# Kernel optimization log

Measured on AMD Instinct MI355X. Metric: run time of the kernel, lower is better.

## Reference

```python
import jax, jax.numpy as jnp
import numpy as np

IN_DIM, H1, H2, N_CLS, N_DOM = 7, 64, 128, 9, 2
N_S, E_S = 100000, 3200000
N_C, E_C = 512, 16384


def gcn_conv(x, edge_index, W, b):
    # PyG GCNConv: x' = D^{-1/2} (A + I) D^{-1/2} (x W) + b
    N = x.shape[0]
    h = x @ W
    loops = jnp.arange(N)
    row = jnp.concatenate([edge_index[0], loops])  # sources
    col = jnp.concatenate([edge_index[1], loops])  # targets
    deg = jax.ops.segment_sum(jnp.ones_like(col, dtype=h.dtype), col, num_segments=N)
    dis = jnp.where(deg > 0, jax.lax.rsqrt(deg), 0.0)
    norm = dis[row] * dis[col]
    out = jax.ops.segment_sum(h[row] * norm[:, None], col, num_segments=N)
    return out + b


def setup_inputs() -> dict:
    key = jax.random.key(0)
    ks = jax.random.split(key, 24)
    d = {}
    d['x_s'] = jax.random.normal(ks[0], (N_S, IN_DIM), dtype=jnp.float32)
    d['x_c'] = jax.random.normal(ks[1], (N_C, IN_DIM), dtype=jnp.float32)
    d['Q'] = jax.random.uniform(ks[2], (N_S, N_C), dtype=jnp.float32)
    d['edge_index_s'] = jax.random.randint(ks[3], (2, E_S), 0, N_S)
    d['edge_index_c'] = jax.random.randint(ks[4], (2, E_C), 0, N_C)
    s = 0.1
    d['W1s'] = jax.random.normal(ks[5], (IN_DIM, H1)) * s
    d['b1s'] = jnp.zeros((H1,), jnp.float32)
    d['W2s'] = jax.random.normal(ks[6], (H1, H2)) * s
    d['b2s'] = jnp.zeros((H2,), jnp.float32)
    d['W1c'] = jax.random.normal(ks[7], (IN_DIM, H1)) * s
    d['b1c'] = jnp.zeros((H1,), jnp.float32)
    d['W2c'] = jax.random.normal(ks[8], (H1, H2)) * s
    d['b2c'] = jnp.zeros((H2,), jnp.float32)
    d['A1'] = jax.random.normal(ks[9], (2 * H2, H2)) * s
    d['ab1'] = jnp.zeros((H2,), jnp.float32)
    d['A2'] = jax.random.normal(ks[10], (H2, 2)) * s
    d['ab2'] = jnp.zeros((2,), jnp.float32)
    d['Wcls'] = jax.random.normal(ks[11], (H2, N_CLS)) * s
    d['bcls'] = jnp.zeros((N_CLS,), jnp.float32)
    d['D1'] = jax.random.normal(ks[12], (H2, H1)) * s
    d['db1'] = jnp.zeros((H1,), jnp.float32)
    d['D2'] = jax.random.normal(ks[13], (H1, N_DOM)) * s
    d['db2'] = jnp.zeros((N_DOM,), jnp.float32)
    return d


def reference(x_s, x_c, Q, edge_index_s, edge_index_c,
              W1s, b1s, W2s, b2s, W1c, b1c, W2c, b2c,
              A1, ab1, A2, ab2, Wcls, bcls, D1, db1, D2, db2):
    # sample branch (eval mode: dropout is identity)
    xs = jax.nn.relu(gcn_conv(x_s, edge_index_s, W1s, b1s))
    xs = jax.nn.relu(gcn_conv(xs, edge_index_s, W2s, b2s))
    # cluster branch
    xc = jax.nn.relu(gcn_conv(x_c, edge_index_c, W1c, b1c))
    xc = jax.nn.relu(gcn_conv(xc, edge_index_c, W2c, b2c))
    # cross-graph decode
    xc_dec = Q @ xc  # [N_s, 128]
    fusion = jnp.concatenate([xs, xc_dec], axis=1)  # [N_s, 256]
    w = jax.nn.softmax(jax.nn.relu(fusion @ A1 + ab1) @ A2 + ab2, axis=1)
    fused = w[:, 0:1] * xs + w[:, 1:2] * xc_dec
    class_output = fused @ Wcls + bcls
    # gradient reversal is identity in forward
    domain_output = jax.nn.relu(fused @ D1 + db1) @ D2 + db2
    return (class_output, domain_output, fused)
```

## Files before the change

### kernel.cpp

```cpp
#include <hip/hip_runtime.h>
#include <cstdint>
#include <cstddef>

static constexpr int kNS = 100000;
static constexpr int kNC = 512;
static constexpr int kES = 3200000;
static constexpr int kEC = 16384;

static constexpr int kNB = (kNS + 63) / 64;
static constexpr int kNB8 = kNB * 8;
static constexpr int kCHUNK = 8192;
static constexpr int kNBLK = (kES + kCHUNK - 1) / kCHUNK;

static constexpr int kGemmQBlocks = (kNS + 63) / 64;
static constexpr int kAgg64Blocks = (kNS + 7) / 8;
static constexpr int kG1 = 625;
static constexpr int kG2 = 469;
static constexpr int kG3 = kGemmQBlocks - kG1 - kG2;

typedef __attribute__((ext_vector_type(8))) short short8;
typedef __attribute__((ext_vector_type(4))) float f32x4;

__device__ __forceinline__ unsigned short f2bf(float f) {
  union { float f; unsigned u; } v; v.f = f;
  unsigned u = v.u;
  unsigned r = (u + 0x7fffu + ((u >> 16) & 1u)) >> 16;
  return (unsigned short)r;
}
__device__ __forceinline__ float bflo(unsigned v) { return __uint_as_float(v << 16); }
__device__ __forceinline__ float bfhi(unsigned v) { return __uint_as_float(v & 0xffff0000u); }
__device__ __forceinline__ float bf2f(unsigned short s) { return __uint_as_float(((unsigned)s) << 16); }

__global__ __launch_bounds__(256) void k_passA(const int* __restrict__ col, int E,
                                               int* __restrict__ counts) {
  __shared__ int hist[kNB];
  int t = threadIdx.x, bid = blockIdx.x;
  for (int j = t; j < kNB; j += 256) hist[j] = 0;
  __syncthreads();
  int base = bid * kCHUNK;
#pragma unroll 4
  for (int i = 0; i < kCHUNK / 256; i++) {
    int e = base + i * 256 + t;
    if (e < E) atomicAdd(&hist[col[e] >> 6], 1);
  }
  __syncthreads();
  int sub = bid & 7;
  for (int j = t; j < kNB; j += 256) {
    int v = hist[j];
    if (v) atomicAdd(&counts[j * 8 + sub], v);
  }
}

__global__ void k_scan_flat(const int* __restrict__ cnt, int n, int* __restrict__ starts,
                            int* __restrict__ cursor, float* __restrict__ dis) {
  __shared__ int s[256];
  int t = threadIdx.x;
  int run = 0;
  for (int base = 0; base < n; base += 256) {
    int i = base + t;
    int v = (i < n) ? cnt[i] : 0;
    s[t] = v;
    __syncthreads();
    for (int o = 1; o < 256; o <<= 1) {
      int x = (t >= o) ? s[t - o] : 0;
      __syncthreads();
      s[t] += x;
      __syncthreads();
    }
    if (i < n) {
      int ex = run + s[t] - v;
      starts[i] = ex;
      cursor[i] = ex;
      if (dis) dis[i] = rsqrtf((float)(v + 1));
    }
    int tot = s[255];
    __syncthreads();
    run += tot;
  }
  if (t == 0) starts[n] = run;
}

__device__ __forceinline__ void passB_body(int bid, int t, const int* __restrict__ row,
                                           const int* __restrict__ col, int E,
                                           int* __restrict__ cursor, unsigned* __restrict__ edg) {
  __shared__ int hist[kNB];
  int sub = bid & 7;
  for (int j = t; j < kNB; j += 256) hist[j] = 0;
  __syncthreads();
  int base = bid * kCHUNK;
#pragma unroll 4
  for (int i = 0; i < kCHUNK / 256; i++) {
    int e = base + i * 256 + t;
    if (e < E) atomicAdd(&hist[col[e] >> 6], 1);
  }
  __syncthreads();
  for (int j = t; j < kNB; j += 256) {
    int v = hist[j];
    hist[j] = v ? atomicAdd(&cursor[j * 8 + sub], v) : 0;
  }
  __syncthreads();
#pragma unroll 4
  for (int i = 0; i < kCHUNK / 256; i++) {
    int e = base + i * 256 + t;
    if (e < E) {
      int c = col[e];
      int pos = atomicAdd(&hist[c >> 6], 1);
      edg[pos] = ((unsigned)row[e] << 6) | (unsigned)(c & 63);
    }
  }
}

__device__ __forceinline__ void passC_body(int b, int t, const unsigned* __restrict__ edg,
                                           const int* __restrict__ bstarts,
                                           int* __restrict__ deg, int* __restrict__ nstarts,
                                           float* __restrict__ dis, int* __restrict__ srow,
                                           const float* __restrict__ x, unsigned* __restrict__ z, int N) {
  __shared__ int ldeg[64];
  __shared__ int lcur[64];
  int s0 = bstarts[b * 8], s1 = bstarts[b * 8 + 8];
  if (t < 64) ldeg[t] = 0;
  __syncthreads();
  for (int i = s0 + t; i < s1; i += 256) atomicAdd(&ldeg[edg[i] & 63u], 1);
  __syncthreads();
  if (t < 64) {
    int own = ldeg[t];
    int incl = own;
#pragma unroll
    for (int off = 1; off < 64; off <<= 1) {
      int o = __shfl_up(incl, off);
      if (t >= off) incl += o;
    }
    int st = s0 + incl - own;
    lcur[t] = st;
    int g = b * 64 + t;
    if (g < N) {
      deg[g] = own;
      nstarts[g] = st;
      float d = rsqrtf((float)(own + 1));
      dis[g] = d;
      const float* xr = x + (size_t)g * 7;
      unsigned w0 = (unsigned)f2bf(xr[0] * d) | ((unsigned)f2bf(xr[1] * d) << 16);
      unsigned w1 = (unsigned)f2bf(xr[2] * d) | ((unsigned)f2bf(xr[3] * d) << 16);
      unsigned w2 = (unsigned)f2bf(xr[4] * d) | ((unsigned)f2bf(xr[5] * d) << 16);
      unsigned w3 = (unsigned)f2bf(xr[6] * d);
      uint4 o = {w0, w1, w2, w3};
      *(uint4*)(z + (size_t)g * 4) = o;
    }
  }
  __syncthreads();
  for (int i = s0 + t; i < s1; i += 256) {
    unsigned ew = edg[i];
    int pos = atomicAdd(&lcur[ew & 63u], 1);
    srow[pos] = (int)(ew >> 6);
  }
}

__global__ void k_hist(const int* __restrict__ col, int E, int* __restrict__ cnt) {
  int i = blockIdx.x * blockDim.x + threadIdx.x;
  if (i < E) atomicAdd(&cnt[col[i]], 1);
}

__global__ void k_scatter(const int* __restrict__ row, const int* __restrict__ col, int E,
                          int* __restrict__ cursor, int* __restrict__ srow) {
  int i = blockIdx.x * blockDim.x + threadIdx.x;
  if (i < E) {
    int pos = atomicAdd(&cursor[col[i]], 1);
    srow[pos] = row[i];
  }
}

__global__ __launch_bounds__(256) void k_z(const float* __restrict__ x, const float* __restrict__ dis,
                                           unsigned* __restrict__ z, int N) {
  int r = blockIdx.x * 256 + threadIdx.x;
  if (r >= N) return;
  const float* xr = x + (size_t)r * 7;
  float d = dis[r];
  unsigned w0 = (unsigned)f2bf(xr[0] * d) | ((unsigned)f2bf(xr[1] * d) << 16);
  unsigned w1 = (unsigned)f2bf(xr[2] * d) | ((unsigned)f2bf(xr[3] * d) << 16);
  unsigned w2 = (unsigned)f2bf(xr[4] * d) | ((unsigned)f2bf(xr[5] * d) << 16);
  unsigned w3 = (unsigned)f2bf(xr[6] * d);
  uint4 o = {w0, w1, w2, w3};
  *(uint4*)(z + (size_t)r * 4) = o;
}

__global__ __launch_bounds__(256) void k_agg7(const unsigned* __restrict__ z,
                                              const int* __restrict__ starts, const int* __restrict__ cnt,
                                              const int* __restrict__ srow, const float* __restrict__ dis,
                                              unsigned* __restrict__ a7, int N) {
  int c = blockIdx.x * 256 + threadIdx.x;
  if (c >= N) return;
  uint4 v = *(const uint4*)(z + (size_t)c * 4);
  float a0 = bflo(v.x), a1 = bfhi(v.x), a2 = bflo(v.y), a3 = bfhi(v.y);
  float a4 = bflo(v.z), a5 = bfhi(v.z), a6 = bflo(v.w), a7v = bfhi(v.w);
  int s0 = starts[c], n = cnt[c];
  const int* sp = srow + s0;
  int e = 0;
  for (; e + 4 <= n; e += 4) {
    uint4 w0 = *(const uint4*)(z + (size_t)sp[e] * 4);
    uint4 w1 = *(const uint4*)(z + (size_t)sp[e + 1] * 4);
    uint4 w2 = *(const uint4*)(z + (size_t)sp[e + 2] * 4);
    uint4 w3 = *(const uint4*)(z + (size_t)sp[e + 3] * 4);
    a0 += bflo(w0.x) + bflo(w1.x) + bflo(w2.x) + bflo(w3.x);
    a1 += bfhi(w0.x) + bfhi(w1.x) + bfhi(w2.x) + bfhi(w3.x);
    a2 += bflo(w0.y) + bflo(w1.y) + bflo(w2.y) + bflo(w3.y);
    a3 += bfhi(w0.y) + bfhi(w1.y) + bfhi(w2.y) + bfhi(w3.y);
    a4 += bflo(w0.z) + bflo(w1.z) + bflo(w2.z) + bflo(w3.z);
    a5 += bfhi(w0.z) + bfhi(w1.z) + bfhi(w2.z) + bfhi(w3.z);
    a6 += bflo(w0.w) + bflo(w1.w) + bflo(w2.w) + bflo(w3.w);
    a7v += bfhi(w0.w) + bfhi(w1.w) + bfhi(w2.w) + bfhi(w3.w);
  }
  for (; e < n; e++) {
    uint4 w = *(const uint4*)(z + (size_t)sp[e] * 4);
    a0 += bflo(w.x); a1 += bfhi(w.x); a2 += bflo(w.y); a3 += bfhi(w.y);
    a4 += bflo(w.z); a5 += bfhi(w.z); a6 += bflo(w.w); a7v += bfhi(w.w);
  }
  float d = dis[c];
  unsigned o0 = (unsigned)f2bf(a0 * d) | ((unsigned)f2bf(a1 * d) << 16);
  unsigned o1 = (unsigned)f2bf(a2 * d) | ((unsigned)f2bf(a3 * d) << 16);
  unsigned o2 = (unsigned)f2bf(a4 * d) | ((unsigned)f2bf(a5 * d) << 16);
  unsigned o3 = (unsigned)f2bf(a6 * d) | ((unsigned)f2bf(a7v * d) << 16);
  uint4 o = {o0, o1, o2, o3};
  *(uint4*)(a7 + (size_t)c * 4) = o;
}

__global__ __launch_bounds__(256) void k_lin7b(const unsigned* __restrict__ a7, const float* __restrict__ W,
                                               const float* __restrict__ b, const float* __restrict__ dis,
                                               unsigned short* __restrict__ y, int N) {
  __shared__ float Ws[7 * 64];
  int t = threadIdx.x;
  for (int j = t; j < 7 * 64; j += 256) Ws[j] = W[j];
  __syncthreads();
  int idx = blockIdx.x * 256 + t;
  if (idx < N * 32) {
    int r = idx >> 5, c2 = (idx & 31) * 2;
    uint4 v = *(const uint4*)(a7 + (size_t)r * 4);
    float a[7] = {bflo(v.x), bfhi(v.x), bflo(v.y), bfhi(v.y), bflo(v.z), bfhi(v.z), bflo(v.w)};
    float s0 = b[c2], s1 = b[c2 + 1];
#pragma unroll
    for (int k = 0; k < 7; k++) {
      s0 = fmaf(a[k], Ws[k * 64 + c2], s0);
      s1 = fmaf(a[k], Ws[k * 64 + c2 + 1], s1);
    }
    float d = dis[r];
    float y0 = fmaxf(s0, 0.f) * d;
    float y1 = fmaxf(s1, 0.f) * d;
    *(unsigned*)(y + (size_t)r * 64 + c2) = (unsigned)f2bf(y0) | ((unsigned)f2bf(y1) << 16);
  }
}

__device__ __forceinline__ void agg64_body(int bid, int t,
                                           const unsigned short* __restrict__ ys,
                                           const int* __restrict__ starts, const int* __restrict__ cnt,
                                           const int* __restrict__ srow, const float* __restrict__ dis,
                                           unsigned short* __restrict__ out, int N) {
  constexpr int F = 64, LPN = 32;
  int c = bid * (256 / LPN) + t / LPN;
  if (c >= N) return;
  int fi = (t % LPN) * 2;
  unsigned v = *(const unsigned*)(ys + (size_t)c * F + fi);
  float ax = bflo(v), ay = bfhi(v);
  int s0 = starts[c], n = cnt[c];
  const int* sp = srow + s0;
  int e = 0;
  for (; e + 8 <= n; e += 8) {
    int r0 = sp[e], r1 = sp[e + 1], r2 = sp[e + 2], r3 = sp[e + 3];
    int r4 = sp[e + 4], r5 = sp[e + 5], r6 = sp[e + 6], r7 = sp[e + 7];
    unsigned v0 = *(const unsigned*)(ys + (size_t)r0 * F + fi);
    unsigned v1 = *(const unsigned*)(ys + (size_t)r1 * F + fi);
    unsigned v2 = *(const unsigned*)(ys + (size_t)r2 * F + fi);
    unsigned v3 = *(const unsigned*)(ys + (size_t)r3 * F + fi);
    unsigned v4 = *(const unsigned*)(ys + (size_t)r4 * F + fi);
    unsigned v5 = *(const unsigned*)(ys + (size_t)r5 * F + fi);
    unsigned v6 = *(const unsigned*)(ys + (size_t)r6 * F + fi);
    unsigned v7 = *(const unsigned*)(ys + (size_t)r7 * F + fi);
    ax += bflo(v0) + bflo(v1) + bflo(v2) + bflo(v3) + bflo(v4) + bflo(v5) + bflo(v6) + bflo(v7);
    ay += bfhi(v0) + bfhi(v1) + bfhi(v2) + bfhi(v3) + bfhi(v4) + bfhi(v5) + bfhi(v6) + bfhi(v7);
  }
  for (; e + 4 <= n; e += 4) {
    int r0 = sp[e], r1 = sp[e + 1], r2 = sp[e + 2], r3 = sp[e + 3];
    unsigned v0 = *(const unsigned*)(ys + (size_t)r0 * F + fi);
    unsigned v1 = *(const unsigned*)(ys + (size_t)r1 * F + fi);
    unsigned v2 = *(const unsigned*)(ys + (size_t)r2 * F + fi);
    unsigned v3 = *(const unsigned*)(ys + (size_t)r3 * F + fi);
    ax += bflo(v0) + bflo(v1) + bflo(v2) + bflo(v3);
    ay += bfhi(v0) + bfhi(v1) + bfhi(v2) + bfhi(v3);
  }
  for (; e < n; e++) {
    unsigned vv = *(const unsigned*)(ys + (size_t)sp[e] * F + fi);
    ax += bflo(vv);
    ay += bfhi(vv);
  }
  float d = dis[c];
  *(unsigned*)(out + (size_t)c * F + fi) = (unsigned)f2bf(ax * d) | ((unsigned)f2bf(ay * d) << 16);
}

__global__ __launch_bounds__(256) void k_agg64(const unsigned short* __restrict__ ys,
                                               const int* __restrict__ starts, const int* __restrict__ cnt,
                                               const int* __restrict__ srow, const float* __restrict__ dis,
                                               unsigned short* __restrict__ out, int N) {
  agg64_body(blockIdx.x, threadIdx.x, ys, starts, cnt, srow, dis, out, N);
}

__global__ __launch_bounds__(256) void k_lin64x128(const unsigned short* __restrict__ xin, const float* __restrict__ W,
                                                   const float* __restrict__ b, unsigned short* __restrict__ hs, int N) {
  __shared__ float Ws[64 * 128];
  __shared__ float xs[32][64];
  int t = threadIdx.x;
  for (int j = t; j < 64 * 128; j += 256) Ws[j] = W[j];
  int r0 = blockIdx.x * 32;
  for (int j = t; j < 32 * 64; j += 256) {
    int r = j >> 6, k = j & 63;
    int gr = r0 + r;
    xs[r][k] = (gr < N) ? bf2f(xin[(size_t)gr * 64 + k]) : 0.f;
  }
  __syncthreads();
  int c = t & 63;
  int rb = (t >> 6) * 8;
  float a0[8], a1[8];
#pragma unroll
  for (int rr = 0; rr < 8; rr++) { a0[rr] = 0.f; a1[rr] = 0.f; }
  for (int k = 0; k < 64; k++) {
    float w0 = Ws[k * 128 + c];
    float w1 = Ws[k * 128 + c + 64];
#pragma unroll
    for (int rr = 0; rr < 8; rr++) {
      float xv = xs[rb + rr][k];
      a0[rr] = fmaf(xv, w0, a0[rr]);
      a1[rr] = fmaf(xv, w1, a1[rr]);
    }
  }
  float bb0 = b[c], bb1 = b[c + 64];
#pragma unroll
  for (int rr = 0; rr < 8; rr++) {
    int gr = r0 + rb + rr;
    if (gr < N) {
      hs[(size_t)gr * 128 + c] = f2bf(fmaxf(a0[rr] + bb0, 0.f));
      hs[(size_t)gr * 128 + c + 64] = f2bf(fmaxf(a1[rr] + bb1, 0.f));
    }
  }
}

__global__ void k_pack_all(const unsigned short* __restrict__ xc2b, const float* __restrict__ A1,
                           const float* __restrict__ D1, const float* __restrict__ Wcls,
                           short* __restrict__ Bq, short* __restrict__ A1p, short* __restrict__ Bh) {
  int i = blockIdx.x * 256 + threadIdx.x;
  if (i < 512 * 128) {
    int e = i;
    int k = e >> 7, n = e & 127;
    int frag = (k >> 5) * 8 + (n >> 4);
    int l = (n & 15) | (((k >> 3) & 3) << 4);
    int j = k & 7;
    Bq[(size_t)frag * 512 + l * 8 + j] = (short)xc2b[e];
  } else if (i < 512 * 128 + 256 * 128) {
    int e = i - 512 * 128;
    int k = e >> 7, n = e & 127;
    int frag = (k >> 5) * 8 + (n >> 4);
    int l = (n & 15) | (((k >> 3) & 3) << 4);
    int j = k & 7;
    A1p[(size_t)frag * 512 + l * 8 + j] = (short)f2bf(A1[e]);
  } else if (i < 512 * 128 + 256 * 128 + 128 * 80) {
    int e = i - (512 * 128 + 256 * 128);
    int k = e / 80, n = e % 80;
    float v = 0.f;
    if (n < 64) v = D1[k * 64 + n];
    else if (n < 73) v = Wcls[k * 9 + (n - 64)];
    int frag = (k >> 5) * 5 + (n >> 4);
    int l = (n & 15) | (((k >> 3) & 3) << 4);
    int j = k & 7;
    Bh[(size_t)frag * 512 + l * 8 + j] = (short)f2bf(v);
  }
}

__device__ __forceinline__ short8 zero8() {
  short8 z;
#pragma unroll
  for (int j = 0; j < 8; j++) z[j] = 0;
  return z;
}

__device__ __forceinline__ short8 cvt8(float4 v0, float4 v1) {
  short8 r;
  r[0] = (short)f2bf(v0.x); r[1] = (short)f2bf(v0.y); r[2] = (short)f2bf(v0.z); r[3] = (short)f2bf(v0.w);
  r[4] = (short)f2bf(v1.x); r[5] = (short)f2bf(v1.y); r[6] = (short)f2bf(v1.z); r[7] = (short)f2bf(v1.w);
  return r;
}

__device__ __forceinline__ short8 load_a_f32(const float* p, bool ok) {
  if (!ok) return zero8();
  return cvt8(*(const float4*)p, *(const float4*)(p + 4));
}

__device__ __forceinline__ void gemm_q_body(int bid, int t, const float* __restrict__ Q,
                                            const short* __restrict__ Bp,
                                            unsigned short* __restrict__ outb, int M) {
  int lane = t & 63;
  int wid = t >> 6;
  int m0 = bid * 64 + wid * 16;
  int mrow = lane & 15;
  int kg = lane >> 4;
  f32x4 acc[8];
#pragma unroll
  for (int nf = 0; nf < 8; nf++) acc[nf] = (f32x4){0.f, 0.f, 0.f, 0.f};
  int r0 = m0 + mrow;
  bool ok = r0 < M;
  const float* ap = Q + (size_t)r0 * 512 + kg * 8;
  const short* bl = Bp + lane * 8;
  float4 z4 = {0.f, 0.f, 0.f, 0.f};
  float4 v0 = ok ? *(const float4*)ap : z4;
  float4 v1 = ok ? *(const float4*)(ap + 4) : z4;
  for (int ks = 0; ks < 16; ks++) {
    float4 n0 = z4, n1 = z4;
    if (ks < 15 && ok) {
      n0 = *(const float4*)(ap + (ks + 1) * 32);
      n1 = *(const float4*)(ap + (ks + 1) * 32 + 4);
    }
    short8 a = cvt8(v0, v1);
    const short* bb = bl + (ks << 12);
#pragma unroll
    for (int nf = 0; nf < 8; nf++) {
      short8 b = *(const short8*)(bb + (nf << 9));
      acc[nf] = __builtin_amdgcn_mfma_f32_16x16x32_bf16(a, b, acc[nf], 0, 0, 0);
    }
    v0 = n0;
    v1 = n1;
  }
  int col = lane & 15;
  int g = lane >> 4;
#pragma unroll
  for (int nf = 0; nf < 8; nf++)
#pragma unroll
    for (int r = 0; r < 4; r++) {
      int row = m0 + g * 4 + r;
      if (row < M) outb[(size_t)row * 128 + nf * 16 + col] = f2bf(acc[nf][r]);
    }
}

__global__ __launch_bounds__(256) void k_fatB(const float* __restrict__ Q, const short* __restrict__ Bq,
                                              unsigned short* __restrict__ xcdb, int M,
                                              const int* __restrict__ row, const int* __restrict__ col, int E,
                                              int* __restrict__ cursor, unsigned* __restrict__ edg) {
  int bid = blockIdx.x, t = threadIdx.x;
  if (bid < kG1) gemm_q_body(bid, t, Q, Bq, xcdb, M);
  else passB_body(bid - kG1, t, row, col, E, cursor, edg);
}

__global__ __launch_bounds__(256) void k_fatC(const float* __restrict__ Q, const short* __restrict__ Bq,
                                              unsigned short* __restrict__ xcdb, int M,
                                              const unsigned* __restrict__ edg, const int* __restrict__ bstarts,
                                              int* __restrict__ deg, int* __restrict__ nstarts,
                                              float* __restrict__ dis, int* __restrict__ srow,
                                              const float* __restrict__ xs, unsigned* __restrict__ zs) {
  int bid = blockIdx.x, t = threadIdx.x;
  if (bid < kG2) gemm_q_body(kG1 + bid, t, Q, Bq, xcdb, M);
  else passC_body(bid - kG2, t, edg, bstarts, deg, nstarts, dis, srow, xs, zs, M);
}

__global__ __launch_bounds__(256) void k_fatA(const float* __restrict__ Q, const short* __restrict__ Bq,
                                              unsigned short* __restrict__ xcdb,
                                              const unsigned short* __restrict__ ys,
                                              const int* __restrict__ starts, const int* __restrict__ cnt,
                                              const int* __restrict__ srow, const float* __restrict__ dis,
                                              unsigned short* __restrict__ gt, int M) {
  int bid = blockIdx.x, t = threadIdx.x;
  if (bid < kG3) gemm_q_body(kG1 + kG2 + bid, t, Q, Bq, xcdb, M);
  else agg64_body(bid - kG3, t, ys, starts, cnt, srow, dis, gt, M);
}

__global__ __launch_bounds__(256) void k_gemm_fuse_mfma(const unsigned short* __restrict__ Xs,
                                                        const unsigned short* __restrict__ Xc,
                                                        const short* __restrict__ A1p, const float* __restrict__ ab1,
                                                        const float* __restrict__ A2, const float* __restrict__ ab2,
                                                        float* __restrict__ fused, int M) {
  int t = threadIdx.x;
  int lane = t & 63;
  int wid = t >> 6;
  int m0 = blockIdx.x * 64 + wid * 16;
  int mrow = lane & 15;
  int kg = lane >> 4;
  f32x4 acc[8];
#pragma unroll
  for (int nf = 0; nf < 8; nf++) acc[nf] = (f32x4){0.f, 0.f, 0.f, 0.f};
  int r0 = m0 + mrow;
  bool ok = r0 < M;
  const short* bl = A1p + lane * 8;
  short8 a = ok ? *(const short8*)(Xs + (size_t)r0 * 128 + kg * 8) : zero8();
  for (int ks = 0; ks < 8; ks++) {
    short8 an = zero8();
    if (ks < 7 && ok) {
      int ks1 = ks + 1;
      const unsigned short* src = (ks1 < 4) ? Xs : Xc;
      an = *(const short8*)(src + (size_t)r0 * 128 + (ks1 & 3) * 32 + kg * 8);
    }
    const short* bb = bl + (ks << 12);
#pragma unroll
    for (int nf = 0; nf < 8; nf++) {
      short8 b = *(const short8*)(bb + (nf << 9));
      acc[nf] = __builtin_amdgcn_mfma_f32_16x16x32_bf16(a, b, acc[nf], 0, 0, 0);
    }
    a = an;
  }
  int col16 = lane & 15;
  int g = lane >> 4;
  float bias[8], w20[8], w21[8];
#pragma unroll
  for (int nf = 0; nf < 8; nf++) {
    int cc = nf * 16 + col16;
    bias[nf] = ab1[cc];
    w20[nf] = A2[2 * cc];
    w21[nf] = A2[2 * cc + 1];
  }
  float b20 = ab2[0], b21 = ab2[1];
#pragma unroll
  for (int r = 0; r < 4; r++) {
    float u0 = 0.f, u1 = 0.f;
#pragma unroll
    for (int nf = 0; nf < 8; nf++) {
      float tv = fmaxf(acc[nf][r] + bias[nf], 0.f);
      u0 = fmaf(tv, w20[nf], u0);
      u1 = fmaf(tv, w21[nf], u1);
    }
#pragma unroll
    for (int off = 1; off < 16; off <<= 1) {
      u0 += __shfl_xor(u0, off);
      u1 += __shfl_xor(u1, off);
    }
    int row = m0 + g * 4 + r;
    if (row < M) {
      float ua = u0 + b20, ub = u1 + b21;
      float mx = fmaxf(ua, ub);
      float e0 = __expf(ua - mx), e1 = __expf(ub - mx);
      float inv = 1.f / (e0 + e1);
      float w0 = e0 * inv, w1 = e1 * inv;
      int p = col16;
      const unsigned short* xsp = Xs + (size_t)row * 128 + p * 8;
      const unsigned short* xcp = Xc + (size_t)row * 128 + p * 8;
      float* op = fused + (size_t)row * 128 + p * 8;
      float4 o0, o1;
      unsigned sx0 = *(const unsigned*)(xsp + 0), sx1 = *(const unsigned*)(xsp + 2);
      unsigned sx2 = *(const unsigned*)(xsp + 4), sx3 = *(const unsigned*)(xsp + 6);
      unsigned cx0 = *(const unsigned*)(xcp + 0), cx1 = *(const unsigned*)(xcp + 2);
      unsigned cx2 = *(const unsigned*)(xcp + 4), cx3 = *(const unsigned*)(xcp + 6);
      o0.x = w0 * bflo(sx0) + w1 * bflo(cx0);
      o0.y = w0 * bfhi(sx0) + w1 * bfhi(cx0);
      o0.z = w0 * bflo(sx1) + w1 * bflo(cx1);
      o0.w = w0 * bfhi(sx1) + w1 * bfhi(cx1);
      o1.x = w0 * bflo(sx2) + w1 * bflo(cx2);
      o1.y = w0 * bfhi(sx2) + w1 * bfhi(cx2);
      o1.z = w0 * bflo(sx3) + w1 * bflo(cx3);
      o1.w = w0 * bfhi(sx3) + w1 * bfhi(cx3);
      *(float4*)op = o0;
      *(float4*)(op + 4) = o1;
    }
  }
}

__global__ __launch_bounds__(256) void k_final_mfma(const float* __restrict__ fused, const short* __restrict__ Bh,
                                                    const float* __restrict__ bcls, const float* __restrict__ db1,
                                                    const float* __restrict__ D2, const float* __restrict__ db2,
                                                    float* __restrict__ cls_out, float* __restrict__ dom_out, int M) {
  int t = threadIdx.x;
  int lane = t & 63;
  int wid = t >> 6;
  int m0 = blockIdx.x * 128 + wid * 32;
  int mrow = lane & 15;
  int kg = lane >> 4;
  f32x4 acc[2][5];
#pragma unroll
  for (int mi = 0; mi < 2; mi++)
#pragma unroll
    for (int nf = 0; nf < 5; nf++) acc[mi][nf] = (f32x4){0.f, 0.f, 0.f, 0.f};
  int r0 = m0 + mrow, r1 = m0 + 16 + mrow;
  bool ok0 = r0 < M, ok1 = r1 < M;
  const float* a0p = fused + (size_t)r0 * 128 + kg * 8;
  const float* a1p = fused + (size_t)r1 * 128 + kg * 8;
  const short* bl = Bh + lane * 8;
  for (int ks = 0; ks < 4; ks++) {
    short8 a0 = load_a_f32(a0p + ks * 32, ok0);
    short8 a1 = load_a_f32(a1p + ks * 32, ok1);
    const short* bb = bl + ks * 5 * 512;
#pragma unroll
    for (int nf = 0; nf < 5; nf++) {
      short8 b = *(const short8*)(bb + (nf << 9));
      acc[0][nf] = __builtin_amdgcn_mfma_f32_16x16x32_bf16(a0, b, acc[0][nf], 0, 0, 0);
      acc[1][nf] = __builtin_amdgcn_mfma_f32_16x16x32_bf16(a1, b, acc[1][nf], 0, 0, 0);
    }
  }
  int col16 = lane & 15;
  int g = lane >> 4;
  float bh[4], d20[4], d21[4];
#pragma unroll
  for (int nf = 0; nf < 4; nf++) {
    int h = col16 + 16 * nf;
    bh[nf] = db1[h];
    d20[nf] = D2[h * 2];
    d21[nf] = D2[h * 2 + 1];
  }
  float bc = (col16 < 9) ? bcls[col16] : 0.f;
  float b20 = db2[0], b21 = db2[1];
#pragma unroll
  for (int mi = 0; mi < 2; mi++) {
#pragma unroll
    for (int r = 0; r < 4; r++) {
      float p0 = 0.f, p1 = 0.f;
#pragma unroll
      for (int nf = 0; nf < 4; nf++) {
        float hv = fmaxf(acc[mi][nf][r] + bh[nf], 0.f);
        p0 = fmaf(hv, d20[nf], p0);
        p1 = fmaf(hv, d21[nf], p1);
      }
#pragma unroll
      for (int off = 1; off < 16; off <<= 1) {
        p0 += __shfl_xor(p0, off);
        p1 += __shfl_xor(p1, off);
      }
      int row = m0 + mi * 16 + g * 4 + r;
      if (row < M) {
        if (col16 < 9) cls_out[(size_t)row * 9 + col16] = acc[mi][4][r] + bc;
        if (col16 == 0) {
          dom_out[(size_t)row * 2 + 0] = p0 + b20;
          dom_out[(size_t)row * 2 + 1] = p1 + b21;
        }
      }
    }
  }
}

extern "C" void kernel_launch(void* const* d_in, const int* in_sizes, int n_in,
                              void* d_out, int out_size, void* d_ws, size_t ws_size,
                              hipStream_t stream) {
  const float* x_s = (const float*)d_in[0];
  const float* x_c = (const float*)d_in[1];
  const float* Q = (const float*)d_in[2];
  const int* eis = (const int*)d_in[3];
  const int* eic = (const int*)d_in[4];
  const float* W1s = (const float*)d_in[5];
  const float* b1s = (const float*)d_in[6];
  const float* W2s = (const float*)d_in[7];
  const float* b2s = (const float*)d_in[8];
  const float* W1c = (const float*)d_in[9];
  const float* b1c = (const float*)d_in[10];
  const float* W2c = (const float*)d_in[11];
  const float* b2c = (const float*)d_in[12];
  const float* A1 = (const float*)d_in[13];
  const float* ab1 = (const float*)d_in[14];
  const float* A2 = (const float*)d_in[15];
  const float* ab2 = (const float*)d_in[16];
  const float* Wcls = (const float*)d_in[17];
  const float* bcls = (const float*)d_in[18];
  const float* D1 = (const float*)d_in[19];
  const float* db1 = (const float*)d_in[20];
  const float* D2 = (const float*)d_in[21];
  const float* db2 = (const float*)d_in[22];

  float* out_cls = (float*)d_out;
  float* out_dom = out_cls + (size_t)kNS * 9;
  float* out_fus = out_dom + (size_t)kNS * 2;

  char* p = (char*)d_ws;
  auto alloc = [&](size_t bytes) -> void* {
    void* r = (void*)p;
    p += (bytes + 255) & ~(size_t)255;
    return r;
  };
  int* deg_s = (int*)alloc((size_t)kNS * 4);
  float* dis_s = (float*)alloc((size_t)kNS * 4);
  int* nstarts_s = (int*)alloc((size_t)kNS * 4);
  int* counts_s = (int*)alloc((size_t)kNB8 * 4);
  int* bstarts_s = (int*)alloc((size_t)(kNB8 + 1) * 4);
  int* bcursor_s = (int*)alloc((size_t)kNB8 * 4);
  int* srow_s = (int*)alloc((size_t)kES * 4);
  unsigned* edg_s = (unsigned*)alloc((size_t)kES * 4);
  int* deg_c = (int*)alloc((size_t)kNC * 4);
  int* cstarts_c = (int*)alloc((size_t)(kNC + 1) * 4);
  int* cursor_c = (int*)alloc((size_t)kNC * 4);
  float* dis_c = (float*)alloc((size_t)kNC * 4);
  int* srow_c = (int*)alloc((size_t)kEC * 4);
  unsigned* zs = (unsigned*)alloc((size_t)kNS * 16);
  unsigned* a7s = (unsigned*)alloc((size_t)kNS * 16);
  unsigned short* ys = (unsigned short*)alloc((size_t)kNS * 64 * 2);
  unsigned short* gts = (unsigned short*)alloc((size_t)kNS * 64 * 2);
  unsigned short* xs2b = (unsigned short*)alloc((size_t)kNS * 128 * 2);
  unsigned short* xcdb = (unsigned short*)alloc((size_t)kNS * 128 * 2);
  unsigned* zc = (unsigned*)alloc((size_t)kNC * 16);
  unsigned* a7c = (unsigned*)alloc((size_t)kNC * 16);
  unsigned short* yc = (unsigned short*)alloc((size_t)kNC * 64 * 2);
  unsigned short* gtc = (unsigned short*)alloc((size_t)kNC * 64 * 2);
  unsigned short* xc2b = (unsigned short*)alloc((size_t)kNC * 128 * 2);
  short* Bq = (short*)alloc((size_t)512 * 128 * 2);
  short* A1p = (short*)alloc((size_t)256 * 128 * 2);
  short* Bh = (short*)alloc((size_t)128 * 80 * 2);
  (void)ws_size; (void)in_sizes; (void)n_in; (void)out_size;

  hipMemsetAsync(counts_s, 0, (size_t)kNB8 * 4, stream);
  hipMemsetAsync(deg_c, 0, (size_t)kNC * 4, stream);

  k_passA<<<kNBLK, 256, 0, stream>>>(eis + kES, kES, counts_s);
  k_scan_flat<<<1, 256, 0, stream>>>(counts_s, kNB8, bstarts_s, bcursor_s, nullptr);

  k_hist<<<(kEC + 255) / 256, 256, 0, stream>>>(eic + kEC, kEC, deg_c);
  k_scan_flat<<<1, 256, 0, stream>>>(deg_c, kNC, cstarts_c, cursor_c, dis_c);
  k_scatter<<<(kEC + 255) / 256, 256, 0, stream>>>(eic, eic + kEC, kEC, cursor_c, srow_c);
  k_z<<<(kNC + 255) / 256, 256, 0, stream>>>(x_c, dis_c, zc, kNC);
  k_agg7<<<(kNC + 255) / 256, 256, 0, stream>>>(zc, cstarts_c, deg_c, srow_c, dis_c, a7c, kNC);
  k_lin7b<<<(kNC * 32 + 255) / 256, 256, 0, stream>>>(a7c, W1c, b1c, dis_c, yc, kNC);
  k_agg64<<<(kNC + 7) / 8, 256, 0, stream>>>(yc, cstarts_c, deg_c, srow_c, dis_c, gtc, kNC);
  k_lin64x128<<<(kNC + 31) / 32, 256, 0, stream>>>(gtc, W2c, b2c, xc2b, kNC);
  k_pack_all<<<(512 * 128 + 256 * 128 + 128 * 80 + 255) / 256, 256, 0, stream>>>(xc2b, A1, D1, Wcls, Bq, A1p, Bh);

  k_fatB<<<kG1 + kNBLK, 256, 0, stream>>>(Q, Bq, xcdb, kNS, eis, eis + kES, kES, bcursor_s, edg_s);
  k_fatC<<<kG2 + kNB, 256, 0, stream>>>(Q, Bq, xcdb, kNS, edg_s, bstarts_s, deg_s, nstarts_s, dis_s, srow_s, x_s, zs);

  k_agg7<<<(kNS + 255) / 256, 256, 0, stream>>>(zs, nstarts_s, deg_s, srow_s, dis_s, a7s, kNS);
  k_lin7b<<<(kNS * 32 + 255) / 256, 256, 0, stream>>>(a7s, W1s, b1s, dis_s, ys, kNS);

  k_fatA<<<kG3 + kAgg64Blocks, 256, 0, stream>>>(Q, Bq, xcdb, ys, nstarts_s, deg_s, srow_s, dis_s, gts, kNS);

  k_lin64x128<<<(kNS + 31) / 32, 256, 0, stream>>>(gts, W2s, b2s, xs2b, kNS);

  k_gemm_fuse_mfma<<<(kNS + 63) / 64, 256, 0, stream>>>(xs2b, xcdb, A1p, ab1, A2, ab2, out_fus, kNS);
  k_final_mfma<<<(kNS + 127) / 128, 256, 0, stream>>>(out_fus, Bh, bcls, db1, D2, db2, out_cls, out_dom, kNS);
}
```

Measured before the change: 480.2 us.

## Fuse cluster branch into one block, merge agg7+lin7 and the sample-branch tail kernels

```diff
diff --git a/kernel.cpp b/kernel.cpp
--- a/kernel.cpp
+++ b/kernel.cpp
@@ -18,6 +18,9 @@
 static constexpr int kG2 = 469;
 static constexpr int kG3 = kGemmQBlocks - kG1 - kG2;
 
+static constexpr int kClusterSmemInts = 4608;
+static constexpr int kFat0SmemInts = (kClusterSmemInts > kNB) ? kClusterSmemInts : kNB;
+
 typedef __attribute__((ext_vector_type(8))) short short8;
 typedef __attribute__((ext_vector_type(4))) float f32x4;
 
@@ -30,11 +33,12 @@
 __device__ __forceinline__ float bflo(unsigned v) { return __uint_as_float(v << 16); }
 __device__ __forceinline__ float bfhi(unsigned v) { return __uint_as_float(v & 0xffff0000u); }
 __device__ __forceinline__ float bf2f(unsigned short s) { return __uint_as_float(((unsigned)s) << 16); }
-
-__global__ __launch_bounds__(256) void k_passA(const int* __restrict__ col, int E,
-                                               int* __restrict__ counts) {
-  __shared__ int hist[kNB];
-  int t = threadIdx.x, bid = blockIdx.x;
+__device__ __forceinline__ unsigned pk2(float a, float b) {
+  return (unsigned)f2bf(a) | ((unsigned)f2bf(b) << 16);
+}
+
+__device__ __forceinline__ void passA_body(int bid, int t, const int* __restrict__ col, int E,
+                                           int* __restrict__ counts, int* __restrict__ hist) {
   for (int j = t; j < kNB; j += 256) hist[j] = 0;
   __syncthreads();
   int base = bid * kCHUNK;
@@ -51,8 +55,168 @@
   }
 }
 
+__device__ __forceinline__ void cluster_body(
+    int t, const int* __restrict__ erow, const int* __restrict__ ecol,
+    const float* __restrict__ x_c, const float* __restrict__ W1c, const float* __restrict__ b1c,
+    const float* __restrict__ W2c, const float* __restrict__ b2c,
+    const float* __restrict__ A1, const float* __restrict__ D1, const float* __restrict__ Wcls,
+    const float* __restrict__ W2s,
+    int* __restrict__ srow_c, unsigned short* __restrict__ yc, unsigned short* __restrict__ gtc,
+    unsigned short* __restrict__ xc2b,
+    short* __restrict__ Bq, short* __restrict__ A1p, short* __restrict__ Bh, short* __restrict__ W2sp,
+    int* smem) {
+  int* degL = smem;
+  int* startsL = smem + 512;
+  int* curL = smem + 1024;
+  float* disL = (float*)(smem + 1536);
+  unsigned* zL = (unsigned*)(smem + 2048);
+  float* W1L = (float*)(smem + 4096);
+  float* b1L = W1L + 448;
+
+  for (int i = t; i < 512; i += 256) degL[i] = 0;
+  __syncthreads();
+  for (int e = t; e < kEC; e += 256) atomicAdd(&degL[ecol[e]], 1);
+  __syncthreads();
+  for (int i = t; i < 512; i += 256) startsL[i] = degL[i];
+  __syncthreads();
+  for (int o = 1; o < 512; o <<= 1) {
+    int i0 = t, i1 = t + 256;
+    int v0 = (i0 >= o) ? startsL[i0 - o] : 0;
+    int v1 = (i1 >= o) ? startsL[i1 - o] : 0;
+    __syncthreads();
+    startsL[i0] += v0;
+    startsL[i1] += v1;
+    __syncthreads();
+  }
+  for (int i = t; i < 512; i += 256) {
+    int ex = startsL[i] - degL[i];
+    curL[i] = ex;
+    disL[i] = rsqrtf((float)(degL[i] + 1));
+  }
+  __syncthreads();
+  for (int i = t; i < 512; i += 256) startsL[i] -= degL[i];
+  for (int i = t; i < 448; i += 256) W1L[i] = W1c[i];
+  if (t < 64) b1L[t] = b1c[t];
+  __syncthreads();
+  for (int e = t; e < kEC; e += 256) {
+    int c = ecol[e];
+    int pos = atomicAdd(&curL[c], 1);
+    srow_c[pos] = erow[e];
+  }
+  for (int i = t; i < 512; i += 256) {
+    float d = disL[i];
+    const float* xr = x_c + (size_t)i * 7;
+    zL[i * 4 + 0] = pk2(xr[0] * d, xr[1] * d);
+    zL[i * 4 + 1] = pk2(xr[2] * d, xr[3] * d);
+    zL[i * 4 + 2] = pk2(xr[4] * d, xr[5] * d);
+    zL[i * 4 + 3] = (unsigned)f2bf(xr[6] * d);
+  }
+  __syncthreads();
+  for (int c = t; c < 512; c += 256) {
+    float a[7];
+    {
+      unsigned w0 = zL[c * 4], w1 = zL[c * 4 + 1], w2 = zL[c * 4 + 2], w3 = zL[c * 4 + 3];
+      a[0] = bflo(w0); a[1] = bfhi(w0); a[2] = bflo(w1); a[3] = bfhi(w1);
+      a[4] = bflo(w2); a[5] = bfhi(w2); a[6] = bflo(w3);
+    }
+    int s0 = startsL[c], n = degL[c];
+    for (int e = 0; e < n; e++) {
+      int r = srow_c[s0 + e];
+      unsigned w0 = zL[r * 4], w1 = zL[r * 4 + 1], w2 = zL[r * 4 + 2], w3 = zL[r * 4 + 3];
+      a[0] += bflo(w0); a[1] += bfhi(w0); a[2] += bflo(w1); a[3] += bfhi(w1);
+      a[4] += bflo(w2); a[5] += bfhi(w2); a[6] += bflo(w3);
+    }
+    float d = disL[c];
+#pragma unroll
+    for (int k = 0; k < 7; k++) a[k] *= d;
+    for (int j = 0; j < 64; j += 2) {
+      float s0v = b1L[j], s1v = b1L[j + 1];
+#pragma unroll
+      for (int k = 0; k < 7; k++) {
+        s0v = fmaf(a[k], W1L[k * 64 + j], s0v);
+        s1v = fmaf(a[k], W1L[k * 64 + j + 1], s1v);
+      }
+      *(unsigned*)(yc + (size_t)c * 64 + j) = pk2(fmaxf(s0v, 0.f) * d, fmaxf(s1v, 0.f) * d);
+    }
+  }
+  __syncthreads();
+  for (int it = 0; it < 64; it++) {
+    int c = it * 8 + (t >> 5);
+    int fi = (t & 31) * 2;
+    unsigned v = *(const unsigned*)(yc + (size_t)c * 64 + fi);
+    float ax = bflo(v), ay = bfhi(v);
+    int s0 = startsL[c], n = degL[c];
+    for (int e = 0; e < n; e++) {
+      unsigned vv = *(const unsigned*)(yc + (size_t)srow_c[s0 + e] * 64 + fi);
+      ax += bflo(vv);
+      ay += bfhi(vv);
+    }
+    float d = disL[c];
+    *(unsigned*)(gtc + (size_t)c * 64 + fi) = pk2(ax * d, ay * d);
+  }
+  __syncthreads();
+  for (int idx = t; idx < 512 * 64; idx += 256) {
+    int r = idx >> 6, c2 = (idx & 63) * 2;
+    float s0v = b2c[c2], s1v = b2c[c2 + 1];
+    for (int k = 0; k < 64; k++) {
+      float gv = bf2f(gtc[(size_t)r * 64 + k]);
+      s0v = fmaf(gv, W2c[k * 128 + c2], s0v);
+      s1v = fmaf(gv, W2c[k * 128 + c2 + 1], s1v);
+    }
+    *(unsigned*)(xc2b + (size_t)r * 128 + c2) = pk2(fmaxf(s0v, 0.f), fmaxf(s1v, 0.f));
+  }
+  __syncthreads();
+  for (int e = t; e < 512 * 128; e += 256) {
+    int k = e >> 7, n = e & 127;
+    int frag = (k >> 5) * 8 + (n >> 4);
+    int l = (n & 15) | (((k >> 3) & 3) << 4);
+    Bq[(size_t)frag * 512 + l * 8 + (k & 7)] = (short)xc2b[e];
+  }
+  for (int e = t; e < 256 * 128; e += 256) {
+    int k = e >> 7, n = e & 127;
+    int frag = (k >> 5) * 8 + (n >> 4);
+    int l = (n & 15) | (((k >> 3) & 3) << 4);
+    A1p[(size_t)frag * 512 + l * 8 + (k & 7)] = (short)f2bf(A1[e]);
+  }
+  for (int e = t; e < 128 * 80; e += 256) {
+    int k = e / 80, n = e % 80;
+    float v = 0.f;
+    if (n < 64) v = D1[k * 64 + n];
+    else if (n < 73) v = Wcls[k * 9 + (n - 64)];
+    int frag = (k >> 5) * 5 + (n >> 4);
+    int l = (n & 15) | (((k >> 3) & 3) << 4);
+    Bh[(size_t)frag * 512 + l * 8 + (k & 7)] = (short)f2bf(v);
+  }
+  for (int e = t; e < 64 * 128; e += 256) {
+    int k = e >> 7, n = e & 127;
+    int frag = (k >> 5) * 8 + (n >> 4);
+    int l = (n & 15) | (((k >> 3) & 3) << 4);
+    W2sp[(size_t)frag * 512 + l * 8 + (k & 7)] = (short)f2bf(W2s[e]);
+  }
+}
+
+__global__ __launch_bounds__(256) void k_fat0(
+    const int* __restrict__ erow_c, const int* __restrict__ ecol_c,
+    const float* __restrict__ x_c, const float* __restrict__ W1c, const float* __restrict__ b1c,
+    const float* __restrict__ W2c, const float* __restrict__ b2c,
+    const float* __restrict__ A1, const float* __restrict__ D1, const float* __restrict__ Wcls,
+    const float* __restrict__ W2s,
+    int* __restrict__ srow_c, unsigned short* __restrict__ yc, unsigned short* __restrict__ gtc,
+    unsigned short* __restrict__ xc2b,
+    short* __restrict__ Bq, short* __restrict__ A1p, short* __restrict__ Bh, short* __restrict__ W2sp,
+    const int* __restrict__ scol, int E, int* __restrict__ counts) {
+  __shared__ int smem[kFat0SmemInts];
+  int bid = blockIdx.x, t = threadIdx.x;
+  if (bid == 0) {
+    cluster_body(t, erow_c, ecol_c, x_c, W1c, b1c, W2c, b2c, A1, D1, Wcls, W2s,
+                 srow_c, yc, gtc, xc2b, Bq, A1p, Bh, W2sp, smem);
+  } else {
+    passA_body(bid - 1, t, scol, E, counts, smem);
+  }
+}
+
 __global__ void k_scan_flat(const int* __restrict__ cnt, int n, int* __restrict__ starts,
-                            int* __restrict__ cursor, float* __restrict__ dis) {
+                            int* __restrict__ cursor) {
   __shared__ int s[256];
   int t = threadIdx.x;
   int run = 0;
@@ -71,7 +235,6 @@
       int ex = run + s[t] - v;
       starts[i] = ex;
       cursor[i] = ex;
-      if (dis) dis[i] = rsqrtf((float)(v + 1));
     }
     int tot = s[255];
     __syncthreads();
@@ -139,12 +302,9 @@
       float d = rsqrtf((float)(own + 1));
       dis[g] = d;
       const float* xr = x + (size_t)g * 7;
-      unsigned w0 = (unsigned)f2bf(xr[0] * d) | ((unsigned)f2bf(xr[1] * d) << 16);
-      unsigned w1 = (unsigned)f2bf(xr[2] * d) | ((unsigned)f2bf(xr[3] * d) << 16);
-      unsigned w2 = (unsigned)f2bf(xr[4] * d) | ((unsigned)f2bf(xr[5] * d) << 16);
-      unsigned w3 = (unsigned)f2bf(xr[6] * d);
-      uint4 o = {w0, w1, w2, w3};
-      *(uint4*)(z + (size_t)g * 4) = o;
+      uint4 o4 = {pk2(xr[0] * d, xr[1] * d), pk2(xr[2] * d, xr[3] * d),
+                  pk2(xr[4] * d, xr[5] * d), (unsigned)f2bf(xr[6] * d)};
+      *(uint4*)(z + (size_t)g * 4) = o4;
     }
   }
   __syncthreads();
@@ -152,99 +312,6 @@
     unsigned ew = edg[i];
     int pos = atomicAdd(&lcur[ew & 63u], 1);
     srow[pos] = (int)(ew >> 6);
-  }
-}
-
-__global__ void k_hist(const int* __restrict__ col, int E, int* __restrict__ cnt) {
-  int i = blockIdx.x * blockDim.x + threadIdx.x;
-  if (i < E) atomicAdd(&cnt[col[i]], 1);
-}
-
-__global__ void k_scatter(const int* __restrict__ row, const int* __restrict__ col, int E,
-                          int* __restrict__ cursor, int* __restrict__ srow) {
-  int i = blockIdx.x * blockDim.x + threadIdx.x;
-  if (i < E) {
-    int pos = atomicAdd(&cursor[col[i]], 1);
-    srow[pos] = row[i];
-  }
-}
-
-__global__ __launch_bounds__(256) void k_z(const float* __restrict__ x, const float* __restrict__ dis,
-                                           unsigned* __restrict__ z, int N) {
-  int r = blockIdx.x * 256 + threadIdx.x;
-  if (r >= N) return;
-  const float* xr = x + (size_t)r * 7;
-  float d = dis[r];
-  unsigned w0 = (unsigned)f2bf(xr[0] * d) | ((unsigned)f2bf(xr[1] * d) << 16);
-  unsigned w1 = (unsigned)f2bf(xr[2] * d) | ((unsigned)f2bf(xr[3] * d) << 16);
-  unsigned w2 = (unsigned)f2bf(xr[4] * d) | ((unsigned)f2bf(xr[5] * d) << 16);
-  unsigned w3 = (unsigned)f2bf(xr[6] * d);
-  uint4 o = {w0, w1, w2, w3};
-  *(uint4*)(z + (size_t)r * 4) = o;
-}
-
-__global__ __launch_bounds__(256) void k_agg7(const unsigned* __restrict__ z,
-                                              const int* __restrict__ starts, const int* __restrict__ cnt,
-                                              const int* __restrict__ srow, const float* __restrict__ dis,
-                                              unsigned* __restrict__ a7, int N) {
-  int c = blockIdx.x * 256 + threadIdx.x;
-  if (c >= N) return;
-  uint4 v = *(const uint4*)(z + (size_t)c * 4);
-  float a0 = bflo(v.x), a1 = bfhi(v.x), a2 = bflo(v.y), a3 = bfhi(v.y);
-  float a4 = bflo(v.z), a5 = bfhi(v.z), a6 = bflo(v.w), a7v = bfhi(v.w);
-  int s0 = starts[c], n = cnt[c];
-  const int* sp = srow + s0;
-  int e = 0;
-  for (; e + 4 <= n; e += 4) {
-    uint4 w0 = *(const uint4*)(z + (size_t)sp[e] * 4);
-    uint4 w1 = *(const uint4*)(z + (size_t)sp[e + 1] * 4);
-    uint4 w2 = *(const uint4*)(z + (size_t)sp[e + 2] * 4);
-    uint4 w3 = *(const uint4*)(z + (size_t)sp[e + 3] * 4);
-    a0 += bflo(w0.x) + bflo(w1.x) + bflo(w2.x) + bflo(w3.x);
-    a1 += bfhi(w0.x) + bfhi(w1.x) + bfhi(w2.x) + bfhi(w3.x);
-    a2 += bflo(w0.y) + bflo(w1.y) + bflo(w2.y) + bflo(w3.y);
-    a3 += bfhi(w0.y) + bfhi(w1.y) + bfhi(w2.y) + bfhi(w3.y);
-    a4 += bflo(w0.z) + bflo(w1.z) + bflo(w2.z) + bflo(w3.z);
-    a5 += bfhi(w0.z) + bfhi(w1.z) + bfhi(w2.z) + bfhi(w3.z);
-    a6 += bflo(w0.w) + bflo(w1.w) + bflo(w2.w) + bflo(w3.w);
-    a7v += bfhi(w0.w) + bfhi(w1.w) + bfhi(w2.w) + bfhi(w3.w);
-  }
-  for (; e < n; e++) {
-    uint4 w = *(const uint4*)(z + (size_t)sp[e] * 4);
-    a0 += bflo(w.x); a1 += bfhi(w.x); a2 += bflo(w.y); a3 += bfhi(w.y);
-    a4 += bflo(w.z); a5 += bfhi(w.z); a6 += bflo(w.w); a7v += bfhi(w.w);
-  }
-  float d = dis[c];
-  unsigned o0 = (unsigned)f2bf(a0 * d) | ((unsigned)f2bf(a1 * d) << 16);
-  unsigned o1 = (unsigned)f2bf(a2 * d) | ((unsigned)f2bf(a3 * d) << 16);
-  unsigned o2 = (unsigned)f2bf(a4 * d) | ((unsigned)f2bf(a5 * d) << 16);
-  unsigned o3 = (unsigned)f2bf(a6 * d) | ((unsigned)f2bf(a7v * d) << 16);
-  uint4 o = {o0, o1, o2, o3};
-  *(uint4*)(a7 + (size_t)c * 4) = o;
-}
-
-__global__ __launch_bounds__(256) void k_lin7b(const unsigned* __restrict__ a7, const float* __restrict__ W,
-                                               const float* __restrict__ b, const float* __restrict__ dis,
-                                               unsigned short* __restrict__ y, int N) {
-  __shared__ float Ws[7 * 64];
-  int t = threadIdx.x;
-  for (int j = t; j < 7 * 64; j += 256) Ws[j] = W[j];
-  __syncthreads();
-  int idx = blockIdx.x * 256 + t;
-  if (idx < N * 32) {
-    int r = idx >> 5, c2 = (idx & 31) * 2;
-    uint4 v = *(const uint4*)(a7 + (size_t)r * 4);
-    float a[7] = {bflo(v.x), bfhi(v.x), bflo(v.y), bfhi(v.y), bflo(v.z), bfhi(v.z), bflo(v.w)};
-    float s0 = b[c2], s1 = b[c2 + 1];
-#pragma unroll
-    for (int k = 0; k < 7; k++) {
-      s0 = fmaf(a[k], Ws[k * 64 + c2], s0);
-      s1 = fmaf(a[k], Ws[k * 64 + c2 + 1], s1);
-    }
-    float d = dis[r];
-    float y0 = fmaxf(s0, 0.f) * d;
-    float y1 = fmaxf(s1, 0.f) * d;
-    *(unsigned*)(y + (size_t)r * 64 + c2) = (unsigned)f2bf(y0) | ((unsigned)f2bf(y1) << 16);
   }
 }
 
@@ -291,83 +358,69 @@
     ay += bfhi(vv);
   }
   float d = dis[c];
-  *(unsigned*)(out + (size_t)c * F + fi) = (unsigned)f2bf(ax * d) | ((unsigned)f2bf(ay * d) << 16);
-}
-
-__global__ __launch_bounds__(256) void k_agg64(const unsigned short* __restrict__ ys,
-                                               const int* __restrict__ starts, const int* __restrict__ cnt,
-                                               const int* __restrict__ srow, const float* __restrict__ dis,
-                                               unsigned short* __restrict__ out, int N) {
-  agg64_body(blockIdx.x, threadIdx.x, ys, starts, cnt, srow, dis, out, N);
-}
-
-__global__ __launch_bounds__(256) void k_lin64x128(const unsigned short* __restrict__ xin, const float* __restrict__ W,
-                                                   const float* __restrict__ b, unsigned short* __restrict__ hs, int N) {
-  __shared__ float Ws[64 * 128];
-  __shared__ float xs[32][64];
+  *(unsigned*)(out + (size_t)c * F + fi) = pk2(ax * d, ay * d);
+}
+
+__global__ __launch_bounds__(256) void k_agg7lin(const unsigned* __restrict__ z,
+                                                 const int* __restrict__ starts, const int* __restrict__ cnt,
+                                                 const int* __restrict__ srow, const float* __restrict__ dis,
+                                                 const float* __restrict__ W1, const float* __restrict__ b1,
+                                                 unsigned short* __restrict__ y, int N) {
+  __shared__ float WL[7 * 64];
+  __shared__ float bL[64];
   int t = threadIdx.x;
-  for (int j = t; j < 64 * 128; j += 256) Ws[j] = W[j];
-  int r0 = blockIdx.x * 32;
-  for (int j = t; j < 32 * 64; j += 256) {
-    int r = j >> 6, k = j & 63;
-    int gr = r0 + r;
-    xs[r][k] = (gr < N) ? bf2f(xin[(size_t)gr * 64 + k]) : 0.f;
-  }
-  __syncthreads();
-  int c = t & 63;
-  int rb = (t >> 6) * 8;
-  float a0[8], a1[8];
-#pragma unroll
-  for (int rr = 0; rr < 8; rr++) { a0[rr] = 0.f; a1[rr] = 0.f; }
-  for (int k = 0; k < 64; k++) {
-    float w0 = Ws[k * 128 + c];
-    float w1 = Ws[k * 128 + c + 64];
-#pragma unroll
-    for (int rr = 0; rr < 8; rr++) {
-      float xv = xs[rb + rr][k];
-      a0[rr] = fmaf(xv, w0, a0[rr]);
-      a1[rr] = fmaf(xv, w1, a1[rr]);
-    }
-  }
-  float bb0 = b[c], bb1 = b[c + 64];
-#pragma unroll
-  for (int rr = 0; rr < 8; rr++) {
-    int gr = r0 + rb + rr;
-    if (gr < N) {
-      hs[(size_t)gr * 128 + c] = f2bf(fmaxf(a0[rr] + bb0, 0.f));
-      hs[(size_t)gr * 128 + c + 64] = f2bf(fmaxf(a1[rr] + bb1, 0.f));
-    }
-  }
-}
-
-__global__ void k_pack_all(const unsigned short* __restrict__ xc2b, const float* __restrict__ A1,
-                           const float* __restrict__ D1, const float* __restrict__ Wcls,
-                           short* __restrict__ Bq, short* __restrict__ A1p, short* __restrict__ Bh) {
-  int i = blockIdx.x * 256 + threadIdx.x;
-  if (i < 512 * 128) {
-    int e = i;
-    int k = e >> 7, n = e & 127;
-    int frag = (k >> 5) * 8 + (n >> 4);
-    int l = (n & 15) | (((k >> 3) & 3) << 4);
-    int j = k & 7;
-    Bq[(size_t)frag * 512 + l * 8 + j] = (short)xc2b[e];
-  } else if (i < 512 * 128 + 256 * 128) {
-    int e = i - 512 * 128;
-    int k = e >> 7, n = e & 127;
-    int frag = (k >> 5) * 8 + (n >> 4);
-    int l = (n & 15) | (((k >> 3) & 3) << 4);
-    int j = k & 7;
-    A1p[(size_t)frag * 512 + l * 8 + j] = (short)f2bf(A1[e]);
-  } else if (i < 512 * 128 + 256 * 128 + 128 * 80) {
-    int e = i - (512 * 128 + 256 * 128);
-    int k = e / 80, n = e % 80;
-    float v = 0.f;
-    if (n < 64) v = D1[k * 64 + n];
-    else if (n < 73) v = Wcls[k * 9 + (n - 64)];
-    int frag = (k >> 5) * 5 + (n >> 4);
-    int l = (n & 15) | (((k >> 3) & 3) << 4);
-    int j = k & 7;
-    Bh[(size_t)frag * 512 + l * 8 + j] = (short)f2bf(v);
+  for (int j = t; j < 448; j += 256) WL[j] = W1[j];
+  if (t < 64) bL[t] = b1[t];
+  __syncthreads();
+  int c = blockIdx.x * 256 + t;
+  if (c >= N) return;
+  float a[7];
+  {
+    uint4 v = *(const uint4*)(z + (size_t)c * 4);
+    a[0] = bflo(v.x); a[1] = bfhi(v.x); a[2] = bflo(v.y); a[3] = bfhi(v.y);
+    a[4] = bflo(v.z); a[5] = bfhi(v.z); a[6] = bflo(v.w);
+  }
+  int s0 = starts[c], n = cnt[c];
+  const int* sp = srow + s0;
+  int e = 0;
+  for (; e + 4 <= n; e += 4) {
+    uint4 w0 = *(const uint4*)(z + (size_t)sp[e] * 4);
+    uint4 w1 = *(const uint4*)(z + (size_t)sp[e + 1] * 4);
+    uint4 w2 = *(const uint4*)(z + (size_t)sp[e + 2] * 4);
+    uint4 w3 = *(const uint4*)(z + (size_t)sp[e + 3] * 4);
+    a[0] += bflo(w0.x) + bflo(w1.x) + bflo(w2.x) + bflo(w3.x);
+    a[1] += bfhi(w0.x) + bfhi(w1.x) + bfhi(w2.x) + bfhi(w3.x);
+    a[2] += bflo(w0.y) + bflo(w1.y) + bflo(w2.y) + bflo(w3.y);
+    a[3] += bfhi(w0.y) + bfhi(w1.y) + bfhi(w2.y) + bfhi(w3.y);
+    a[4] += bflo(w0.z) + bflo(w1.z) + bflo(w2.z) + bflo(w3.z);
+    a[5] += bfhi(w0.z) + bfhi(w1.z) + bfhi(w2.z) + bfhi(w3.z);
+    a[6] += bflo(w0.w) + bflo(w1.w) + bflo(w2.w) + bflo(w3.w);
+  }
+  for (; e < n; e++) {
+    uint4 w = *(const uint4*)(z + (size_t)sp[e] * 4);
+    a[0] += bflo(w.x); a[1] += bfhi(w.x); a[2] += bflo(w.y); a[3] += bfhi(w.y);
+    a[4] += bflo(w.z); a[5] += bfhi(w.z); a[6] += bflo(w.w);
+  }
+  float d = dis[c];
+#pragma unroll
+  for (int k = 0; k < 7; k++) a[k] *= d;
+  unsigned ow[32];
+#pragma unroll
+  for (int j2 = 0; j2 < 32; j2++) {
+    int j = j2 * 2;
+    float s0v = bL[j], s1v = bL[j + 1];
+#pragma unroll
+    for (int k = 0; k < 7; k++) {
+      s0v = fmaf(a[k], WL[k * 64 + j], s0v);
+      s1v = fmaf(a[k], WL[k * 64 + j + 1], s1v);
+    }
+    ow[j2] = pk2(fmaxf(s0v, 0.f) * d, fmaxf(s1v, 0.f) * d);
+  }
+  uint4* op = (uint4*)(y + (size_t)c * 64);
+#pragma unroll
+  for (int q = 0; q < 8; q++) {
+    uint4 v = {ow[q * 4], ow[q * 4 + 1], ow[q * 4 + 2], ow[q * 4 + 3]};
+    op[q] = v;
   }
 }
 
@@ -383,11 +436,6 @@
   r[0] = (short)f2bf(v0.x); r[1] = (short)f2bf(v0.y); r[2] = (short)f2bf(v0.z); r[3] = (short)f2bf(v0.w);
   r[4] = (short)f2bf(v1.x); r[5] = (short)f2bf(v1.y); r[6] = (short)f2bf(v1.z); r[7] = (short)f2bf(v1.w);
   return r;
-}
-
-__device__ __forceinline__ short8 load_a_f32(const float* p, bool ok) {
-  if (!ok) return zero8();
-  return cvt8(*(const float4*)p, *(const float4*)(p + 4));
 }
 
 __device__ __forceinline__ void gemm_q_body(int bid, int t, const float* __restrict__ Q,
@@ -466,145 +514,165 @@
   else agg64_body(bid - kG3, t, ys, starts, cnt, srow, dis, gt, M);
 }
 
-__global__ __launch_bounds__(256) void k_gemm_fuse_mfma(const unsigned short* __restrict__ Xs,
-                                                        const unsigned short* __restrict__ Xc,
-                                                        const short* __restrict__ A1p, const float* __restrict__ ab1,
-                                                        const float* __restrict__ A2, const float* __restrict__ ab2,
-                                                        float* __restrict__ fused, int M) {
+__global__ __launch_bounds__(256) void k_tail(const unsigned short* __restrict__ gts,
+                                              const short* __restrict__ W2p, const float* __restrict__ b2,
+                                              const unsigned short* __restrict__ Xc,
+                                              const short* __restrict__ A1p, const float* __restrict__ ab1,
+                                              const float* __restrict__ A2, const float* __restrict__ ab2,
+                                              const short* __restrict__ Bh, const float* __restrict__ bcls,
+                                              const float* __restrict__ db1, const float* __restrict__ D2,
+                                              const float* __restrict__ db2,
+                                              float* __restrict__ fused, float* __restrict__ cls_out,
+                                              float* __restrict__ dom_out, int M) {
+  __shared__ unsigned short xs2L[64 * 128];
+  __shared__ unsigned short fusL[64 * 128];
   int t = threadIdx.x;
   int lane = t & 63;
   int wid = t >> 6;
-  int m0 = blockIdx.x * 64 + wid * 16;
+  int m0 = blockIdx.x * 64;
   int mrow = lane & 15;
   int kg = lane >> 4;
-  f32x4 acc[8];
-#pragma unroll
-  for (int nf = 0; nf < 8; nf++) acc[nf] = (f32x4){0.f, 0.f, 0.f, 0.f};
-  int r0 = m0 + mrow;
+  int rowbase = wid * 16;
+  int r0 = m0 + rowbase + mrow;
   bool ok = r0 < M;
-  const short* bl = A1p + lane * 8;
-  short8 a = ok ? *(const short8*)(Xs + (size_t)r0 * 128 + kg * 8) : zero8();
-  for (int ks = 0; ks < 8; ks++) {
-    short8 an = zero8();
-    if (ks < 7 && ok) {
-      int ks1 = ks + 1;
-      const unsigned short* src = (ks1 < 4) ? Xs : Xc;
-      an = *(const short8*)(src + (size_t)r0 * 128 + (ks1 & 3) * 32 + kg * 8);
-    }
-    const short* bb = bl + (ks << 12);
+  int col16 = mrow, g = kg;
+
+  f32x4 acc1[8];
+#pragma unroll
+  for (int nf = 0; nf < 8; nf++) acc1[nf] = (f32x4){0.f, 0.f, 0.f, 0.f};
+#pragma unroll
+  for (int ks = 0; ks < 2; ks++) {
+    short8 a = ok ? *(const short8*)(gts + (size_t)r0 * 64 + ks * 32 + kg * 8) : zero8();
+    const short* bb = W2p + (size_t)(ks * 8) * 512 + lane * 8;
 #pragma unroll
     for (int nf = 0; nf < 8; nf++) {
       short8 b = *(const short8*)(bb + (nf << 9));
-      acc[nf] = __builtin_amdgcn_mfma_f32_16x16x32_bf16(a, b, acc[nf], 0, 0, 0);
-    }
-    a = an;
-  }
-  int col16 = lane & 15;
-  int g = lane >> 4;
-  float bias[8], w20[8], w21[8];
-#pragma unroll
-  for (int nf = 0; nf < 8; nf++) {
-    int cc = nf * 16 + col16;
-    bias[nf] = ab1[cc];
-    w20[nf] = A2[2 * cc];
-    w21[nf] = A2[2 * cc + 1];
-  }
-  float b20 = ab2[0], b21 = ab2[1];
-#pragma unroll
-  for (int r = 0; r < 4; r++) {
-    float u0 = 0.f, u1 = 0.f;
+      acc1[nf] = __builtin_amdgcn_mfma_f32_16x16x32_bf16(a, b, acc1[nf], 0, 0, 0);
+    }
+  }
+#pragma unroll
+  for (int nf = 0; nf < 8; nf++)
+#pragma unroll
+    for (int r = 0; r < 4; r++) {
+      int col = nf * 16 + col16;
+      int rl = rowbase + g * 4 + r;
+      float v = fmaxf(acc1[nf][r] + b2[col], 0.f);
+      xs2L[rl * 128 + (((col >> 3) ^ (rl & 15)) << 3) + (col & 7)] = f2bf(v);
+    }
+  __syncthreads();
+
+  f32x4 acc2[8];
+#pragma unroll
+  for (int nf = 0; nf < 8; nf++) acc2[nf] = (f32x4){0.f, 0.f, 0.f, 0.f};
+  int rl0 = rowbase + mrow;
+#pragma unroll
+  for (int ks = 0; ks < 8; ks++) {
+    short8 a;
+    if (ks < 4) {
+      int colg = ks * 4 + kg;
+      a = *(const short8*)&xs2L[rl0 * 128 + ((colg ^ mrow) << 3)];
+    } else {
+      a = ok ? *(const short8*)(Xc + (size_t)r0 * 128 + (ks - 4) * 32 + kg * 8) : zero8();
+    }
+    const short* bb = A1p + (size_t)(ks * 8) * 512 + lane * 8;
 #pragma unroll
     for (int nf = 0; nf < 8; nf++) {
-      float tv = fmaxf(acc[nf][r] + bias[nf], 0.f);
-      u0 = fmaf(tv, w20[nf], u0);
-      u1 = fmaf(tv, w21[nf], u1);
-    }
-#pragma unroll
-    for (int off = 1; off < 16; off <<= 1) {
-      u0 += __shfl_xor(u0, off);
-      u1 += __shfl_xor(u1, off);
-    }
-    int row = m0 + g * 4 + r;
-    if (row < M) {
-      float ua = u0 + b20, ub = u1 + b21;
-      float mx = fmaxf(ua, ub);
-      float e0 = __expf(ua - mx), e1 = __expf(ub - mx);
-      float inv = 1.f / (e0 + e1);
-      float w0 = e0 * inv, w1 = e1 * inv;
-      int p = col16;
-      const unsigned short* xsp = Xs + (size_t)row * 128 + p * 8;
-      const unsigned short* xcp = Xc + (size_t)row * 128 + p * 8;
-      float* op = fused + (size_t)row * 128 + p * 8;
-      float4 o0, o1;
-      unsigned sx0 = *(const unsigned*)(xsp + 0), sx1 = *(const unsigned*)(xsp + 2);
-      unsigned sx2 = *(const unsigned*)(xsp + 4), sx3 = *(const unsigned*)(xsp + 6);
-      unsigned cx0 = *(const unsigned*)(xcp + 0), cx1 = *(const unsigned*)(xcp + 2);
-      unsigned cx2 = *(const unsigned*)(xcp + 4), cx3 = *(const unsigned*)(xcp + 6);
-      o0.x = w0 * bflo(sx0) + w1 * bflo(cx0);
-      o0.y = w0 * bfhi(sx0) + w1 * bfhi(cx0);
-      o0.z = w0 * bflo(sx1) + w1 * bflo(cx1);
-      o0.w = w0 * bfhi(sx1) + w1 * bfhi(cx1);
-      o1.x = w0 * bflo(sx2) + w1 * bflo(cx2);
-      o1.y = w0 * bfhi(sx2) + w1 * bfhi(cx2);
-      o1.z = w0 * bflo(sx3) + w1 * bflo(cx3);
-      o1.w = w0 * bfhi(sx3) + w1 * bfhi(cx3);
-      *(float4*)op = o0;
-      *(float4*)(op + 4) = o1;
-    }
-  }
-}
-
-__global__ __launch_bounds__(256) void k_final_mfma(const float* __restrict__ fused, const short* __restrict__ Bh,
-                                                    const float* __restrict__ bcls, const float* __restrict__ db1,
-                                                    const float* __restrict__ D2, const float* __restrict__ db2,
-                                                    float* __restrict__ cls_out, float* __restrict__ dom_out, int M) {
-  int t = threadIdx.x;
-  int lane = t & 63;
-  int wid = t >> 6;
-  int m0 = blockIdx.x * 128 + wid * 32;
-  int mrow = lane & 15;
-  int kg = lane >> 4;
-  f32x4 acc[2][5];
-#pragma unroll
-  for (int mi = 0; mi < 2; mi++)
-#pragma unroll
-    for (int nf = 0; nf < 5; nf++) acc[mi][nf] = (f32x4){0.f, 0.f, 0.f, 0.f};
-  int r0 = m0 + mrow, r1 = m0 + 16 + mrow;
-  bool ok0 = r0 < M, ok1 = r1 < M;
-  const float* a0p = fused + (size_t)r0 * 128 + kg * 8;
-  const float* a1p = fused + (size_t)r1 * 128 + kg * 8;
-  const short* bl = Bh + lane * 8;
+      short8 b = *(const short8*)(bb + (nf << 9));
+      acc2[nf] = __builtin_amdgcn_mfma_f32_16x16x32_bf16(a, b, acc2[nf], 0, 0, 0);
+    }
+  }
+  {
+    float bias[8], w20[8], w21[8];
+#pragma unroll
+    for (int nf = 0; nf < 8; nf++) {
+      int cc = nf * 16 + col16;
+      bias[nf] = ab1[cc];
+      w20[nf] = A2[2 * cc];
+      w21[nf] = A2[2 * cc + 1];
+    }
+    float b20 = ab2[0], b21 = ab2[1];
+#pragma unroll
+    for (int r = 0; r < 4; r++) {
+      float u0 = 0.f, u1 = 0.f;
+#pragma unroll
+      for (int nf = 0; nf < 8; nf++) {
+        float tv = fmaxf(acc2[nf][r] + bias[nf], 0.f);
+        u0 = fmaf(tv, w20[nf], u0);
+        u1 = fmaf(tv, w21[nf], u1);
+      }
+#pragma unroll
+      for (int off = 1; off < 16; off <<= 1) {
+        u0 += __shfl_xor(u0, off);
+        u1 += __shfl_xor(u1, off);
+      }
+      int rl = rowbase + g * 4 + r;
+      int row = m0 + rl;
+      if (row < M) {
+        float ua = u0 + b20, ub = u1 + b21;
+        float mx = fmaxf(ua, ub);
+        float e0 = __expf(ua - mx), e1 = __expf(ub - mx);
+        float inv = 1.f / (e0 + e1);
+        float w0 = e0 * inv, w1 = e1 * inv;
+        int p = col16;
+        const unsigned short* xsp = &xs2L[rl * 128 + ((p ^ (rl & 15)) << 3)];
+        const unsigned short* xcp = Xc + (size_t)row * 128 + p * 8;
+        unsigned short* fp = &fusL[rl * 128 + ((p ^ (rl & 15)) << 3)];
+        float* op = fused + (size_t)row * 128 + p * 8;
+        float4 o0, o1;
+        unsigned cx0 = *(const unsigned*)(xcp + 0), cx1 = *(const unsigned*)(xcp + 2);
+        unsigned cx2 = *(const unsigned*)(xcp + 4), cx3 = *(const unsigned*)(xcp + 6);
+        o0.x = w0 * bf2f(xsp[0]) + w1 * bflo(cx0);
+        o0.y = w0 * bf2f(xsp[1]) + w1 * bfhi(cx0);
+        o0.z = w0 * bf2f(xsp[2]) + w1 * bflo(cx1);
+        o0.w = w0 * bf2f(xsp[3]) + w1 * bfhi(cx1);
+        o1.x = w0 * bf2f(xsp[4]) + w1 * bflo(cx2);
+        o1.y = w0 * bf2f(xsp[5]) + w1 * bfhi(cx2);
+        o1.z = w0 * bf2f(xsp[6]) + w1 * bflo(cx3);
+        o1.w = w0 * bf2f(xsp[7]) + w1 * bfhi(cx3);
+        *(float4*)op = o0;
+        *(float4*)(op + 4) = o1;
+        fp[0] = f2bf(o0.x); fp[1] = f2bf(o0.y); fp[2] = f2bf(o0.z); fp[3] = f2bf(o0.w);
+        fp[4] = f2bf(o1.x); fp[5] = f2bf(o1.y); fp[6] = f2bf(o1.z); fp[7] = f2bf(o1.w);
+      } else {
+        unsigned short* fp = &fusL[rl * 128 + ((col16 ^ (rl & 15)) << 3)];
+#pragma unroll
+        for (int q = 0; q < 8; q++) fp[q] = 0;
+      }
+    }
+  }
+  __syncthreads();
+
+  f32x4 acc3[5];
+#pragma unroll
+  for (int nf = 0; nf < 5; nf++) acc3[nf] = (f32x4){0.f, 0.f, 0.f, 0.f};
+#pragma unroll
   for (int ks = 0; ks < 4; ks++) {
-    short8 a0 = load_a_f32(a0p + ks * 32, ok0);
-    short8 a1 = load_a_f32(a1p + ks * 32, ok1);
-    const short* bb = bl + ks * 5 * 512;
+    int colg = ks * 4 + kg;
+    short8 a = *(const short8*)&fusL[rl0 * 128 + ((colg ^ mrow) << 3)];
+    const short* bb = Bh + (size_t)(ks * 5) * 512 + lane * 8;
 #pragma unroll
     for (int nf = 0; nf < 5; nf++) {
       short8 b = *(const short8*)(bb + (nf << 9));
-      acc[0][nf] = __builtin_amdgcn_mfma_f32_16x16x32_bf16(a0, b, acc[0][nf], 0, 0, 0);
-      acc[1][nf] = __builtin_amdgcn_mfma_f32_16x16x32_bf16(a1, b, acc[1][nf], 0, 0, 0);
-    }
-  }
-  int col16 = lane & 15;
-  int g = lane >> 4;
-  float bh[4], d20[4], d21[4];
-#pragma unroll
-  for (int nf = 0; nf < 4; nf++) {
-    int h = col16 + 16 * nf;
-    bh[nf] = db1[h];
-    d20[nf] = D2[h * 2];
-    d21[nf] = D2[h * 2 + 1];
-  }
-  float bc = (col16 < 9) ? bcls[col16] : 0.f;
-  float b20 = db2[0], b21 = db2[1];
-#pragma unroll
-  for (int mi = 0; mi < 2; mi++) {
+      acc3[nf] = __builtin_amdgcn_mfma_f32_16x16x32_bf16(a, b, acc3[nf], 0, 0, 0);
+    }
+  }
+  {
+    float bh[4], d20[4], d21[4];
+#pragma unroll
+    for (int nf = 0; nf < 4; nf++) {
+      int h = col16 + 16 * nf;
+      bh[nf] = db1[h];
+      d20[nf] = D2[h * 2];
+      d21[nf] = D2[h * 2 + 1];
+    }
+    float bc = (col16 < 9) ? bcls[col16] : 0.f;
+    float b20 = db2[0], b21 = db2[1];
 #pragma unroll
     for (int r = 0; r < 4; r++) {
       float p0 = 0.f, p1 = 0.f;
 #pragma unroll
       for (int nf = 0; nf < 4; nf++) {
-        float hv = fmaxf(acc[mi][nf][r] + bh[nf], 0.f);
+        float hv = fmaxf(acc3[nf][r] + bh[nf], 0.f);
         p0 = fmaf(hv, d20[nf], p0);
         p1 = fmaf(hv, d21[nf], p1);
       }
@@ -613,9 +681,9 @@
         p0 += __shfl_xor(p0, off);
         p1 += __shfl_xor(p1, off);
       }
-      int row = m0 + mi * 16 + g * 4 + r;
+      int row = m0 + rowbase + g * 4 + r;
       if (row < M) {
-        if (col16 < 9) cls_out[(size_t)row * 9 + col16] = acc[mi][4][r] + bc;
+        if (col16 < 9) cls_out[(size_t)row * 9 + col16] = acc3[4][r] + bc;
         if (col16 == 0) {
           dom_out[(size_t)row * 2 + 0] = p0 + b20;
           dom_out[(size_t)row * 2 + 1] = p1 + b21;
@@ -670,53 +738,36 @@
   int* bcursor_s = (int*)alloc((size_t)kNB8 * 4);
   int* srow_s = (int*)alloc((size_t)kES * 4);
   unsigned* edg_s = (unsigned*)alloc((size_t)kES * 4);
-  int* deg_c = (int*)alloc((size_t)kNC * 4);
-  int* cstarts_c = (int*)alloc((size_t)(kNC + 1) * 4);
-  int* cursor_c = (int*)alloc((size_t)kNC * 4);
-  float* dis_c = (float*)alloc((size_t)kNC * 4);
   int* srow_c = (int*)alloc((size_t)kEC * 4);
-  unsigned* zs = (unsigned*)alloc((size_t)kNS * 16);
-  unsigned* a7s = (unsigned*)alloc((size_t)kNS * 16);
-  unsigned short* ys = (unsigned short*)alloc((size_t)kNS * 64 * 2);
-  unsigned short* gts = (unsigned short*)alloc((size_t)kNS * 64 * 2);
-  unsigned short* xs2b = (unsigned short*)alloc((size_t)kNS * 128 * 2);
-  unsigned short* xcdb = (unsigned short*)alloc((size_t)kNS * 128 * 2);
-  unsigned* zc = (unsigned*)alloc((size_t)kNC * 16);
-  unsigned* a7c = (unsigned*)alloc((size_t)kNC * 16);
   unsigned short* yc = (unsigned short*)alloc((size_t)kNC * 64 * 2);
   unsigned short* gtc = (unsigned short*)alloc((size_t)kNC * 64 * 2);
   unsigned short* xc2b = (unsigned short*)alloc((size_t)kNC * 128 * 2);
+  unsigned* zs = (unsigned*)alloc((size_t)kNS * 16);
+  unsigned short* ys = (unsigned short*)alloc((size_t)kNS * 64 * 2);
+  unsigned short* gts = (unsigned short*)alloc((size_t)kNS * 64 * 2);
+  unsigned short* xcdb = (unsigned short*)alloc((size_t)kNS * 128 * 2);
   short* Bq = (short*)alloc((size_t)512 * 128 * 2);
   short* A1p = (short*)alloc((size_t)256 * 128 * 2);
   short* Bh = (short*)alloc((size_t)128 * 80 * 2);
+  short* W2sp = (short*)alloc((size_t)64 * 128 * 2);
   (void)ws_size; (void)in_sizes; (void)n_in; (void)out_size;
 
   hipMemsetAsync(counts_s, 0, (size_t)kNB8 * 4, stream);
-  hipMemsetAsync(deg_c, 0, (size_t)kNC * 4, stream);
-
-  k_passA<<<kNBLK, 256, 0, stream>>>(eis + kES, kES, counts_s);
-  k_scan_flat<<<1, 256, 0, stream>>>(counts_s, kNB8, bstarts_s, bcursor_s, nullptr);
-
-  k_hist<<<(kEC + 255) / 256, 256, 0, stream>>>(eic + kEC, kEC, deg_c);
-  k_scan_flat<<<1, 256, 0, stream>>>(deg_c, kNC, cstarts_c, cursor_c, dis_c);
-  k_scatter<<<(kEC + 255) / 256, 256, 0, stream>>>(eic, eic + kEC, kEC, cursor_c, srow_c);
-  k_z<<<(kNC + 255) / 256, 256, 0, stream>>>(x_c, dis_c, zc, kNC);
-  k_agg7<<<(kNC + 255) / 256, 256, 0, stream>>>(zc, cstarts_c, deg_c, srow_c, dis_c, a7c, kNC);
-  k_lin7b<<<(kNC * 32 + 255) / 256, 256, 0, stream>>>(a7c, W1c, b1c, dis_c, yc, kNC);
-  k_agg64<<<(kNC + 7) / 8, 256, 0, stream>>>(yc, cstarts_c, deg_c, srow_c, dis_c, gtc, kNC);
-  k_lin64x128<<<(kNC + 31) / 32, 256, 0, stream>>>(gtc, W2c, b2c, xc2b, kNC);
-  k_pack_all<<<(512 * 128 + 256 * 128 + 128 * 80 + 255) / 256, 256, 0, stream>>>(xc2b, A1, D1, Wcls, Bq, A1p, Bh);
+
+  k_fat0<<<1 + kNBLK, 256, 0, stream>>>(eic, eic + kEC, x_c, W1c, b1c, W2c, b2c,
+                                        A1, D1, Wcls, W2s,
+                                        srow_c, yc, gtc, xc2b, Bq, A1p, Bh, W2sp,
+                                        eis + kES, kES, counts_s);
+  k_scan_flat<<<1, 256, 0, stream>>>(counts_s, kNB8, bstarts_s, bcursor_s);
 
   k_fatB<<<kG1 + kNBLK, 256, 0, stream>>>(Q, Bq, xcdb, kNS, eis, eis + kES, kES, bcursor_s, edg_s);
   k_fatC<<<kG2 + kNB, 256, 0, stream>>>(Q, Bq, xcdb, kNS, edg_s, bstarts_s, deg_s, nstarts_s, dis_s, srow_s, x_s, zs);
 
-  k_agg7<<<(kNS + 255) / 256, 256, 0, stream>>>(zs, nstarts_s, deg_s, srow_s, dis_s, a7s, kNS);
-  k_lin7b<<<(kNS * 32 + 255) / 256, 256, 0, stream>>>(a7s, W1s, b1s, dis_s, ys, kNS);
+  k_agg7lin<<<(kNS + 255) / 256, 256, 0, stream>>>(zs, nstarts_s, deg_s, srow_s, dis_s, W1s, b1s, ys, kNS);
 
   k_fatA<<<kG3 + kAgg64Blocks, 256, 0, stream>>>(Q, Bq, xcdb, ys, nstarts_s, deg_s, srow_s, dis_s, gts, kNS);
 
-  k_lin64x128<<<(kNS + 31) / 32, 256, 0, stream>>>(gts, W2s, b2s, xs2b, kNS);
-
-  k_gemm_fuse_mfma<<<(kNS + 63) / 64, 256, 0, stream>>>(xs2b, xcdb, A1p, ab1, A2, ab2, out_fus, kNS);
-  k_final_mfma<<<(kNS + 127) / 128, 256, 0, stream>>>(out_fus, Bh, bcls, db1, D2, db2, out_cls, out_dom, kNS);
-}
+  k_tail<<<(kNS + 63) / 64, 256, 0, stream>>>(gts, W2sp, b2s, xcdb, A1p, ab1, A2, ab2,
+                                              Bh, bcls, db1, D2, db2,
+                                              out_fus, out_cls, out_dom, kNS);
+}
```

Measured after the change: 1.311 ms. +172.9%, slower.
